# Optimization experiments

Measured on AMD Instinct MI355X. Metric: run time of the kernel, lower is better.

Reference implementation:

```python
import jax, jax.numpy as jnp
import numpy as np

B, S, A, M = 8, 64, 9, 64          # batch, feature-map side, anchors/pos, max gt boxes
IMG_H, IMG_W = 800.0, 800.0
MATCH_IOU = 0.5                     # match_iou_threshold from __init__


def setup_inputs() -> dict:
    key = jax.random.key(0)
    k1, k2, k3, k4 = jax.random.split(key, 4)
    rpn_bbox_offset_pred = jax.random.normal(k1, (B, S, S, A, 4), jnp.float32) * 0.1
    # second-stage (fast rcnn) offsets for every proposal
    fast_rcnn_offsets = jax.random.normal(k2, (B, S * S * A, 4), jnp.float32) * 0.1
    # valid padded gt boxes in corner format (x1,y1,x2,y2)
    xy = jax.random.uniform(k3, (B, M, 2), jnp.float32, 0.0, 600.0)
    wh = jax.random.uniform(k4, (B, M, 2), jnp.float32, 10.0, 200.0)
    gt_bbox = jnp.concatenate([xy, jnp.minimum(xy + wh, 800.0)], axis=-1)
    # standard 3 scales x 3 ratios anchors
    scales = jnp.array([64.0, 128.0, 256.0], jnp.float32)
    ratios = jnp.array([0.5, 1.0, 2.0], jnp.float32)
    anchor_heights = (scales[:, None] * jnp.sqrt(ratios)[None, :]).reshape(-1)
    anchor_widths = (scales[:, None] / jnp.sqrt(ratios)[None, :]).reshape(-1)
    return dict(rpn_bbox_offset_pred=rpn_bbox_offset_pred,
                fast_rcnn_offsets=fast_rcnn_offsets,
                gt_bbox=gt_bbox,
                anchor_heights=anchor_heights,
                anchor_widths=anchor_widths)


def _decode_rpn(offsets, anchor_h, anchor_w):
    """convert_rpn_bbox_offsets_to_rpn_bbox: anchor-relative offsets -> corner boxes.
    offsets: (B,S,S,A,4) -> (B, S*S*A, 4) clipped to the image."""
    stride_y, stride_x = IMG_H / S, IMG_W / S
    acy = ((jnp.arange(S, dtype=jnp.float32) + 0.5) * stride_y)[:, None, None]  # (S,1,1)
    acx = ((jnp.arange(S, dtype=jnp.float32) + 0.5) * stride_x)[None, :, None]  # (1,S,1)
    ah = anchor_h[None, None, :]  # (1,1,A)
    aw = anchor_w[None, None, :]
    tx, ty, tw, th = offsets[..., 0], offsets[..., 1], offsets[..., 2], offsets[..., 3]
    pcx = acx + tx * aw
    pcy = acy + ty * ah
    pw = aw * jnp.exp(tw)
    ph = ah * jnp.exp(th)
    x1 = jnp.clip(pcx - 0.5 * pw, 0.0, IMG_W)
    y1 = jnp.clip(pcy - 0.5 * ph, 0.0, IMG_H)
    x2 = jnp.clip(pcx + 0.5 * pw, 0.0, IMG_W)
    y2 = jnp.clip(pcy + 0.5 * ph, 0.0, IMG_H)
    return jnp.stack([x1, y1, x2, y2], axis=-1).reshape(offsets.shape[0], -1, 4)


def _box_iou(a, b):
    """torchvision.ops.box_iou: a (N,4), b (M,4) -> (N,M)."""
    area_a = (a[:, 2] - a[:, 0]) * (a[:, 3] - a[:, 1])
    area_b = (b[:, 2] - b[:, 0]) * (b[:, 3] - b[:, 1])
    lt = jnp.maximum(a[:, None, :2], b[None, :, :2])  # (N,M,2)
    rb = jnp.minimum(a[:, None, 2:], b[None, :, 2:])
    wh = jnp.clip(rb - lt, 0.0)
    inter = wh[..., 0] * wh[..., 1]
    return inter / (area_a[:, None] + area_b[None, :] - inter + 1e-9)


def _apply_offsets(boxes, off):
    """apply_offsets_to_fast_rcnn_bbox, exactly as in the torch module."""
    w = boxes[..., 2] - boxes[..., 0]
    h = boxes[..., 3] - boxes[..., 1]
    x1 = off[..., 0] * w + boxes[..., 0]
    y1 = off[..., 1] * h + boxes[..., 1]
    x2 = x1 + jnp.exp(off[..., 2]) * w
    y2 = y1 + jnp.exp(off[..., 3]) * h
    return jnp.stack([x1, y1, x2, y2], axis=-1)


def reference(rpn_bbox_offset_pred, fast_rcnn_offsets, gt_bbox, anchor_heights, anchor_widths):
    # 1. bbox offset decode (anchors -> proposals)
    rpn_bbox_pred = _decode_rpn(rpn_bbox_offset_pred, anchor_heights, anchor_widths)  # (B,N,4)
    # 2. per-image box_iou matching (vectorized over the batch)
    ious = jax.vmap(_box_iou)(rpn_bbox_pred, gt_bbox)  # (B,N,M)
    best_iou = jnp.max(ious, axis=-1)                  # (B,N)
    best_gt_index = jnp.argmax(ious, axis=-1)          # (B,N) int
    is_foreground = best_iou > MATCH_IOU               # rpn_objectness_gt
    # 3. second-stage offset decode on the proposals
    refined_bbox = _apply_offsets(rpn_bbox_pred, fast_rcnn_offsets)  # (B,N,4)
    return rpn_bbox_pred, is_foreground, best_gt_index, refined_bbox
```

## Files before the change

### kernel.cpp

```cpp
#include <hip/hip_runtime.h>

#define BB 8
#define SS 64
#define AA 9
#define MM 64
#define NN (SS * SS * AA)

__global__ __launch_bounds__(256) void frcnn_head_kernel(
    const float* __restrict__ rpn_off,
    const float* __restrict__ frc_off,
    const float* __restrict__ gt,
    const float* __restrict__ anchor_h,
    const float* __restrict__ anchor_w,
    float* __restrict__ out)
{
    __shared__ float gt_s[MM * 4];
    __shared__ float area_s[MM];
    __shared__ float ah_s[AA];
    __shared__ float aw_s[AA];

    const int blocks_per_b = NN / 512;
    const int b     = blockIdx.x / blocks_per_b;
    const int chunk = blockIdx.x % blocks_per_b;
    const int tid   = threadIdx.x;
    const int i0    = chunk * 512 + tid;
    const int i1    = i0 + 256;

    if (tid < MM * 4) gt_s[tid] = gt[(size_t)b * MM * 4 + tid];
    if (tid < AA) { ah_s[tid] = anchor_h[tid]; aw_s[tid] = anchor_w[tid]; }
    __syncthreads();
    if (tid < MM) {
        const float gx1 = gt_s[tid * 4 + 0], gy1 = gt_s[tid * 4 + 1];
        const float gx2 = gt_s[tid * 4 + 2], gy2 = gt_s[tid * 4 + 3];
        area_s[tid] = (gx2 - gx1) * (gy2 - gy1);
    }
    __syncthreads();

    const float stride = 800.0f / (float)SS;
    float bx1[2], by1[2], bx2[2], by2[2], area[2];
    const int ii[2] = { i0, i1 };
    #pragma unroll
    for (int k = 0; k < 2; ++k) {
        const int i     = ii[k];
        const int a_idx = i % AA;
        const int xy    = i / AA;
        const int gx    = xy % SS;
        const int gy    = xy / SS;
        const float acx = ((float)gx + 0.5f) * stride;
        const float acy = ((float)gy + 0.5f) * stride;

        const float4 t = ((const float4*)rpn_off)[(size_t)b * NN + i];
        const float aw = aw_s[a_idx];
        const float ah = ah_s[a_idx];

        const float pcx = acx + t.x * aw;
        const float pcy = acy + t.y * ah;
        const float pw  = aw * expf(t.z);
        const float ph  = ah * expf(t.w);

        bx1[k] = fminf(fmaxf(pcx - 0.5f * pw, 0.0f), 800.0f);
        by1[k] = fminf(fmaxf(pcy - 0.5f * ph, 0.0f), 800.0f);
        bx2[k] = fminf(fmaxf(pcx + 0.5f * pw, 0.0f), 800.0f);
        by2[k] = fminf(fmaxf(pcy + 0.5f * ph, 0.0f), 800.0f);
        area[k] = (bx2[k] - bx1[k]) * (by2[k] - by1[k]);
    }

    float bnum[2] = { -1.0f, -1.0f };
    float bden[2] = {  1.0f,  1.0f };
    int   bj[2]   = {  0, 0 };
    #pragma unroll 4
    for (int j = 0; j < MM; ++j) {
        const float gx1 = gt_s[j * 4 + 0], gy1 = gt_s[j * 4 + 1];
        const float gx2 = gt_s[j * 4 + 2], gy2 = gt_s[j * 4 + 3];
        const float ga  = area_s[j];
        #pragma unroll
        for (int k = 0; k < 2; ++k) {
            const float ix1 = fmaxf(bx1[k], gx1);
            const float iy1 = fmaxf(by1[k], gy1);
            const float ix2 = fminf(bx2[k], gx2);
            const float iy2 = fminf(by2[k], gy2);
            const float iw  = fmaxf(ix2 - ix1, 0.0f);
            const float ih  = fmaxf(iy2 - iy1, 0.0f);
            const float inter = iw * ih;
            const float den   = area[k] + ga - inter + 1e-9f;
            if (inter * bden[k] > bnum[k] * den) {
                bnum[k] = inter; bden[k] = den; bj[k] = j;
            }
        }
    }

    const size_t BN = (size_t)BB * NN;
    const size_t o1 = BN * 4;
    const size_t o2 = o1 + BN;
    const size_t o3 = o2 + BN;

    #pragma unroll
    for (int k = 0; k < 2; ++k) {
        const int i = ii[k];
        const size_t idx = (size_t)b * NN + i;

        const float4 f = ((const float4*)frc_off)[(size_t)b * NN + i];
        const float w = bx2[k] - bx1[k];
        const float h = by2[k] - by1[k];
        const float rx1 = f.x * w + bx1[k];
        const float ry1 = f.y * h + by1[k];
        const float rx2 = rx1 + expf(f.z) * w;
        const float ry2 = ry1 + expf(f.w) * h;

        ((float4*)out)[idx] = make_float4(bx1[k], by1[k], bx2[k], by2[k]);
        out[o1 + idx] = (bnum[k] > 0.5f * bden[k]) ? 1.0f : 0.0f;
        out[o2 + idx] = (float)bj[k];
        ((float4*)(out + o3))[idx] = make_float4(rx1, ry1, rx2, ry2);
    }
}

extern "C" void kernel_launch(void* const* d_in, const int* in_sizes, int n_in,
                              void* d_out, int out_size, void* d_ws, size_t ws_size,
                              hipStream_t stream) {
    const float* rpn_off  = (const float*)d_in[0];
    const float* frc_off  = (const float*)d_in[1];
    const float* gt       = (const float*)d_in[2];
    const float* anchor_h = (const float*)d_in[3];
    const float* anchor_w = (const float*)d_in[4];
    float* out = (float*)d_out;

    const int grid = BB * (NN / 512);
    frcnn_head_kernel<<<grid, 256, 0, stream>>>(rpn_off, frc_off, gt,
                                                anchor_h, anchor_w, out);
}
```

Before: 20.93 us.

## Drop shared-memory staging, split IoU argmax into four chains, use fast exp

```diff
diff --git a/kernel.cpp b/kernel.cpp
--- a/kernel.cpp
+++ b/kernel.cpp
@@ -14,11 +14,6 @@
     const float* __restrict__ anchor_w,
     float* __restrict__ out)
 {
-    __shared__ float gt_s[MM * 4];
-    __shared__ float area_s[MM];
-    __shared__ float ah_s[AA];
-    __shared__ float aw_s[AA];
-
     const int blocks_per_b = NN / 512;
     const int b     = blockIdx.x / blocks_per_b;
     const int chunk = blockIdx.x % blocks_per_b;
@@ -26,18 +21,10 @@
     const int i0    = chunk * 512 + tid;
     const int i1    = i0 + 256;
 
-    if (tid < MM * 4) gt_s[tid] = gt[(size_t)b * MM * 4 + tid];
-    if (tid < AA) { ah_s[tid] = anchor_h[tid]; aw_s[tid] = anchor_w[tid]; }
-    __syncthreads();
-    if (tid < MM) {
-        const float gx1 = gt_s[tid * 4 + 0], gy1 = gt_s[tid * 4 + 1];
-        const float gx2 = gt_s[tid * 4 + 2], gy2 = gt_s[tid * 4 + 3];
-        area_s[tid] = (gx2 - gx1) * (gy2 - gy1);
-    }
-    __syncthreads();
+    const float* __restrict__ gt_b = gt + (size_t)b * MM * 4;
 
     const float stride = 800.0f / (float)SS;
-    float bx1[2], by1[2], bx2[2], by2[2], area[2];
+    float bx1[2], by1[2], bx2[2], by2[2], areaeps[2];
     const int ii[2] = { i0, i1 };
     #pragma unroll
     for (int k = 0; k < 2; ++k) {
@@ -50,44 +37,62 @@
         const float acy = ((float)gy + 0.5f) * stride;
 
         const float4 t = ((const float4*)rpn_off)[(size_t)b * NN + i];
-        const float aw = aw_s[a_idx];
-        const float ah = ah_s[a_idx];
+        const float aw = anchor_w[a_idx];
+        const float ah = anchor_h[a_idx];
 
         const float pcx = acx + t.x * aw;
         const float pcy = acy + t.y * ah;
-        const float pw  = aw * expf(t.z);
-        const float ph  = ah * expf(t.w);
+        const float pw  = aw * __expf(t.z);
+        const float ph  = ah * __expf(t.w);
 
         bx1[k] = fminf(fmaxf(pcx - 0.5f * pw, 0.0f), 800.0f);
         by1[k] = fminf(fmaxf(pcy - 0.5f * ph, 0.0f), 800.0f);
         bx2[k] = fminf(fmaxf(pcx + 0.5f * pw, 0.0f), 800.0f);
         by2[k] = fminf(fmaxf(pcy + 0.5f * ph, 0.0f), 800.0f);
-        area[k] = (bx2[k] - bx1[k]) * (by2[k] - by1[k]);
+        areaeps[k] = (bx2[k] - bx1[k]) * (by2[k] - by1[k]) + 1e-9f;
     }
 
-    float bnum[2] = { -1.0f, -1.0f };
-    float bden[2] = {  1.0f,  1.0f };
-    int   bj[2]   = {  0, 0 };
-    #pragma unroll 4
-    for (int j = 0; j < MM; ++j) {
-        const float gx1 = gt_s[j * 4 + 0], gy1 = gt_s[j * 4 + 1];
-        const float gx2 = gt_s[j * 4 + 2], gy2 = gt_s[j * 4 + 3];
-        const float ga  = area_s[j];
+    float bnum[2][4], bden[2][4];
+    int   bj[2][4];
+    #pragma unroll
+    for (int k = 0; k < 2; ++k)
         #pragma unroll
-        for (int k = 0; k < 2; ++k) {
-            const float ix1 = fmaxf(bx1[k], gx1);
-            const float iy1 = fmaxf(by1[k], gy1);
-            const float ix2 = fminf(bx2[k], gx2);
-            const float iy2 = fminf(by2[k], gy2);
-            const float iw  = fmaxf(ix2 - ix1, 0.0f);
-            const float ih  = fmaxf(iy2 - iy1, 0.0f);
-            const float inter = iw * ih;
-            const float den   = area[k] + ga - inter + 1e-9f;
-            if (inter * bden[k] > bnum[k] * den) {
-                bnum[k] = inter; bden[k] = den; bj[k] = j;
+        for (int c = 0; c < 4; ++c) {
+            bnum[k][c] = -1.0f; bden[k][c] = 1.0f; bj[k][c] = 16 * c;
+        }
+
+    #pragma unroll
+    for (int c = 0; c < 4; ++c) {
+        #pragma unroll 4
+        for (int jc = 0; jc < 16; ++jc) {
+            const int j = c * 16 + jc;
+            const float gx1 = gt_b[j * 4 + 0], gy1 = gt_b[j * 4 + 1];
+            const float gx2 = gt_b[j * 4 + 2], gy2 = gt_b[j * 4 + 3];
+            const float ga  = (gx2 - gx1) * (gy2 - gy1);
+            #pragma unroll
+            for (int k = 0; k < 2; ++k) {
+                const float ix1 = fmaxf(bx1[k], gx1);
+                const float iy1 = fmaxf(by1[k], gy1);
+                const float ix2 = fminf(bx2[k], gx2);
+                const float iy2 = fminf(by2[k], gy2);
+                const float iw  = fmaxf(ix2 - ix1, 0.0f);
+                const float ih  = fmaxf(iy2 - iy1, 0.0f);
+                const float inter = iw * ih;
+                const float den   = (areaeps[k] + ga) - inter;
+                if (inter * bden[k][c] > bnum[k][c] * den) {
+                    bnum[k][c] = inter; bden[k][c] = den; bj[k][c] = j;
+                }
             }
         }
     }
+
+    #pragma unroll
+    for (int k = 0; k < 2; ++k)
+        #pragma unroll
+        for (int c = 1; c < 4; ++c)
+            if (bnum[k][c] * bden[k][0] > bnum[k][0] * bden[k][c]) {
+                bnum[k][0] = bnum[k][c]; bden[k][0] = bden[k][c]; bj[k][0] = bj[k][c];
+            }
 
     const size_t BN = (size_t)BB * NN;
     const size_t o1 = BN * 4;
@@ -104,12 +109,12 @@
         const float h = by2[k] - by1[k];
         const float rx1 = f.x * w + bx1[k];
         const float ry1 = f.y * h + by1[k];
-        const float rx2 = rx1 + expf(f.z) * w;
-        const float ry2 = ry1 + expf(f.w) * h;
+        const float rx2 = rx1 + __expf(f.z) * w;
+        const float ry2 = ry1 + __expf(f.w) * h;
 
         ((float4*)out)[idx] = make_float4(bx1[k], by1[k], bx2[k], by2[k]);
-        out[o1 + idx] = (bnum[k] > 0.5f * bden[k]) ? 1.0f : 0.0f;
-        out[o2 + idx] = (float)bj[k];
+        out[o1 + idx] = (bnum[k][0] > 0.5f * bden[k][0]) ? 1.0f : 0.0f;
+        out[o2 + idx] = (float)bj[k][0];
         ((float4*)(out + o3))[idx] = make_float4(rx1, ry1, rx2, ry2);
     }
 }
```

After: 21.63 us. 3.4% more time.
